# Optimization experiments

Measured on AMD Instinct MI355X. Metric: run time of the kernel, lower is better.

The kernel has to match this reference:

```python
import math
import jax, jax.numpy as jnp
import numpy as np

CHANNELS = 256
NUM_HEADS = 4
GROUPS = 32
EPS = 1e-5


def setup_inputs() -> dict:
    key = jax.random.key(0)
    ks = jax.random.split(key, 7)
    b, c, h, w = 8, CHANNELS, 48, 48
    return {
        "x": jax.random.normal(ks[0], (b, c, h, w), dtype=jnp.float32),
        "gn_w": jax.random.uniform(ks[1], (c,), dtype=jnp.float32),
        "gn_b": jax.random.normal(ks[2], (c,), dtype=jnp.float32) * 0.02,
        "qkv_w": jax.random.normal(ks[3], (3 * c, c), dtype=jnp.float32) * (1.0 / math.sqrt(c)),
        "qkv_b": jax.random.normal(ks[4], (3 * c,), dtype=jnp.float32) * 0.02,
        "proj_w": jax.random.normal(ks[5], (c, c), dtype=jnp.float32) * (1.0 / math.sqrt(c)),
        "proj_b": jax.random.normal(ks[6], (c,), dtype=jnp.float32) * 0.02,
    }


def reference(x, gn_w, gn_b, qkv_w, qkv_b, proj_w, proj_b):
    b, c, h, w = x.shape
    nh = NUM_HEADS
    hd = c // nh
    hw = h * w

    # GroupNorm(32, c): normalize over (c/G, h, w) per group
    xg = x.reshape(b, GROUPS, c // GROUPS, h, w)
    mean = jnp.mean(xg, axis=(2, 3, 4), keepdims=True)
    var = jnp.mean(jnp.square(xg - mean), axis=(2, 3, 4), keepdims=True)
    xn = (xg - mean) * jax.lax.rsqrt(var + EPS)
    xn = xn.reshape(b, c, h, w) * gn_w[None, :, None, None] + gn_b[None, :, None, None]

    # 1x1 conv qkv: per-pixel linear
    qkv = jnp.einsum('bchw,oc->bohw', xn, qkv_w) + qkv_b[None, :, None, None]
    q, k, v = jnp.split(qkv, 3, axis=1)  # each (b, c, h, w)

    # split channels into heads: (b, nh, hd, hw)
    q = q.reshape(b, nh, hd, hw)
    k = k.reshape(b, nh, hd, hw)
    v = v.reshape(b, nh, hd, hw)

    scale = 1.0 / math.sqrt(hd)
    attn = jnp.einsum('bndi,bndj->bnij', q, k) * scale  # (b, nh, hw, hw)
    attn = jax.nn.softmax(attn, axis=-1)
    out = jnp.einsum('bnij,bndj->bndi', attn, v)  # (b, nh, hd, hw)
    out = out.reshape(b, c, h, w)

    out = jnp.einsum('bchw,oc->bohw', out, proj_w) + proj_b[None, :, None, None]
    return x + out
```

## Files before the change

### kernel.cpp

```cpp
#include <hip/hip_runtime.h>
#include <hip/hip_bf16.h>
#include <math.h>

#define NB 8
#define NC 256
#define NHW 2304
#define NH 4
#define HD 64
#define CPG 8
#define GN_EPS 1e-5f

typedef __bf16 bf16;
typedef __bf16 bf16x4 __attribute__((ext_vector_type(4)));
typedef __bf16 bf16x8 __attribute__((ext_vector_type(8)));
typedef float f32x4 __attribute__((ext_vector_type(4)));
typedef float f32x16 __attribute__((ext_vector_type(16)));
typedef int i32x4 __attribute__((ext_vector_type(4)));
typedef unsigned int u32;

#define MFMA16(a, b, c) __builtin_amdgcn_mfma_f32_16x16x32_bf16(a, b, c, 0, 0, 0)
#define MFMA32(a, b, c) __builtin_amdgcn_mfma_f32_32x32x16_bf16(a, b, c, 0, 0, 0)

__global__ __launch_bounds__(256) void k_pre(const float* __restrict__ x,
                                             const float* __restrict__ gw,
                                             const float* __restrict__ gb,
                                             const float* __restrict__ qw,
                                             const float* __restrict__ pw,
                                             bf16* __restrict__ xnt,
                                             bf16* __restrict__ wq,
                                             bf16* __restrict__ wp) {
  int t = threadIdx.x;
  if (blockIdx.x < 768) {
    int i = blockIdx.x * 256 + t;
    wq[i] = (bf16)qw[i];
    if (i < NC * NC) wp[i] = (bf16)pw[i];
    return;
  }
  int bid = blockIdx.x - 768;
  int b = bid >> 5;
  int g = bid & 31;
  int c0 = g * CPG;
  const float* xb = x + (b * NC + c0) * NHW;
  float s = 0.f, s2 = 0.f;
  for (int p = t; p < NHW; p += 256) {
#pragma unroll
    for (int cc = 0; cc < CPG; ++cc) {
      float v = xb[cc * NHW + p];
      s += v;
      s2 += v * v;
    }
  }
#pragma unroll
  for (int m = 1; m < 64; m <<= 1) {
    s += __shfl_xor(s, m);
    s2 += __shfl_xor(s2, m);
  }
  __shared__ float red[8];
  int wid = t >> 6;
  if ((t & 63) == 0) { red[wid] = s; red[4 + wid] = s2; }
  __syncthreads();
  s = red[0] + red[1] + red[2] + red[3];
  s2 = red[4] + red[5] + red[6] + red[7];
  const float inv_n = 1.0f / (CPG * NHW);
  float mean = s * inv_n;
  float var = s2 * inv_n - mean * mean;
  float rsq = rsqrtf(var + GN_EPS);
  float ka[CPG], kb[CPG];
#pragma unroll
  for (int cc = 0; cc < CPG; ++cc) {
    float wv = gw[c0 + cc];
    ka[cc] = wv * rsq;
    kb[cc] = gb[c0 + cc] - mean * rsq * wv;
  }
  bf16* dst = xnt + b * NHW * NC + c0;
  for (int p = t; p < NHW; p += 256) {
    bf16x8 o;
#pragma unroll
    for (int cc = 0; cc < CPG; ++cc)
      o[cc] = (bf16)(xb[cc * NHW + p] * ka[cc] + kb[cc]);
    *reinterpret_cast<bf16x8*>(dst + p * NC) = o;
  }
}

__global__ __launch_bounds__(256) void k_qkv(const bf16* __restrict__ xnt,
                                             const bf16* __restrict__ wq,
                                             const float* __restrict__ qkvb,
                                             bf16* __restrict__ qt,
                                             bf16* __restrict__ kt,
                                             bf16* __restrict__ vv) {
  int b = blockIdx.z;
  int i_base = blockIdx.x * 128;
  int o_base = blockIdx.y * 128;
  int t = threadIdx.x;
  int lane = t & 63, wid = t >> 6;
  int wm = (wid >> 1) * 64, wn = (wid & 1) * 64;
  int l15 = lane & 15, g = lane >> 4;
  const bf16* ab = xnt + (b * NHW + i_base + wm + l15) * NC + g * 8;
  const bf16* bb = wq + (o_base + wn + l15) * NC + g * 8;
  f32x4 acc[4][4] = {};
#pragma unroll 2
  for (int kc = 0; kc < 8; ++kc) {
    bf16x8 af[4], bf[4];
#pragma unroll
    for (int mf = 0; mf < 4; ++mf)
      af[mf] = *reinterpret_cast<const bf16x8*>(ab + mf * 16 * NC + kc * 32);
#pragma unroll
    for (int nf = 0; nf < 4; ++nf)
      bf[nf] = *reinterpret_cast<const bf16x8*>(bb + nf * 16 * NC + kc * 32);
#pragma unroll
    for (int mf = 0; mf < 4; ++mf)
#pragma unroll
      for (int nf = 0; nf < 4; ++nf)
        acc[mf][nf] = MFMA16(af[mf], bf[nf], acc[mf][nf]);
  }
  int row0 = i_base + wm + g * 4;
  if (o_base + wn < 512) {
    const float qscale = 0.125f * 1.4426950408889634f;
#pragma unroll
    for (int nf = 0; nf < 4; ++nf) {
      int o = o_base + wn + nf * 16 + l15;
      float bias = qkvb[o];
      bf16* dst;
      float sc;
      int oo;
      if (o < 256) { dst = qt; sc = qscale; oo = o; }
      else         { dst = kt; sc = 1.0f;   oo = o - 256; }
      bf16* dp = dst + ((b * NH + (oo >> 6)) * NHW) * HD + (oo & 63);
#pragma unroll
      for (int mf = 0; mf < 4; ++mf)
#pragma unroll
        for (int r = 0; r < 4; ++r)
          dp[(row0 + mf * 16 + r) * HD] = (bf16)((acc[mf][nf][r] + bias) * sc);
    }
  } else {
#pragma unroll
    for (int nf = 0; nf < 4; ++nf) {
      int og = o_base + wn + nf * 16 + l15;
      float bias = qkvb[og];
      int o2 = og - 512;
      bf16* dp = vv + ((size_t)(b * NH + (o2 >> 6)) * HD + (o2 & 63)) * NHW +
                 i_base + wm + g * 4;
#pragma unroll
      for (int mf = 0; mf < 4; ++mf) {
        bf16x4 w;
#pragma unroll
        for (int r = 0; r < 4; ++r) w[r] = (bf16)(acc[mf][nf][r] + bias);
        *reinterpret_cast<bf16x4*>(dp + mf * 16) = w;
      }
    }
  }
}

__global__ __launch_bounds__(256) void k_attn(const bf16* __restrict__ qt,
                                              const bf16* __restrict__ kt,
                                              const bf16* __restrict__ vv,
                                              bf16* __restrict__ att) {
  __shared__ bf16 kbuf[2][64 * 64];
  __shared__ bf16 vbuf[2][64 * 64];

  const int bh = blockIdx.y;
  const int b = bh >> 2, n = bh & 3;
  const int tid = threadIdx.x;
  const int wid = tid >> 6, lane = tid & 63;
  const int l31 = lane & 31, g2 = lane >> 5;
  const int i0w = blockIdx.x * 128 + wid * 32;

  const bf16* qb = qt + (size_t)bh * NHW * HD;
  const bf16* kb = kt + (size_t)bh * NHW * HD;
  const bf16* vb = vv + (size_t)bh * HD * NHW;

  const int r0 = tid >> 3, cs = tid & 7;
  const bf16* kg0 = kb + r0 * HD + cs * 8;
  const bf16* kg1 = kb + (r0 + 32) * HD + cs * 8;
  const bf16* vg0 = vb + (size_t)r0 * NHW + cs * 8;
  const bf16* vg1 = vb + (size_t)(r0 + 32) * NHW + cs * 8;
  const int lw0 = r0 * 64 + ((cs ^ (r0 & 7)) * 8);
  const int lw1 = (r0 + 32) * 64 + ((cs ^ (r0 & 7)) * 8);

  const int foff = l31 * 64;
  int sw[4];
#pragma unroll
  for (int m = 0; m < 4; ++m) sw[m] = ((2 * m + g2) ^ (l31 & 7)) * 8;

  bf16x8 q[4];
#pragma unroll
  for (int kk = 0; kk < 4; ++kk)
    q[kk] = *reinterpret_cast<const bf16x8*>(qb + (i0w + l31) * HD + kk * 16 + g2 * 8);

  f32x16 acc0 = {}, acc1 = {};
  float l_r = 0.f;

  {
    bf16x8 a = *reinterpret_cast<const bf16x8*>(kg0);
    bf16x8 c = *reinterpret_cast<const bf16x8*>(kg1);
    bf16x8 d = *reinterpret_cast<const bf16x8*>(vg0);
    bf16x8 e = *reinterpret_cast<const bf16x8*>(vg1);
    *reinterpret_cast<bf16x8*>(&kbuf[0][lw0]) = a;
    *reinterpret_cast<bf16x8*>(&kbuf[0][lw1]) = c;
    *reinterpret_cast<bf16x8*>(&vbuf[0][lw0]) = d;
    *reinterpret_cast<bf16x8*>(&vbuf[0][lw1]) = e;
  }
  asm volatile("s_waitcnt lgkmcnt(0)" ::: "memory");
  __builtin_amdgcn_s_barrier();

  for (int t = 0; t < 36; ++t) {
    const int cur = t & 1;
    bf16x8 kr0, kr1, vr0, vr1;
    if (t < 35) {
      kr0 = *reinterpret_cast<const bf16x8*>(kg0 + (t + 1) * (64 * HD));
      kr1 = *reinterpret_cast<const bf16x8*>(kg1 + (t + 1) * (64 * HD));
      vr0 = *reinterpret_cast<const bf16x8*>(vg0 + (t + 1) * 64);
      vr1 = *reinterpret_cast<const bf16x8*>(vg1 + (t + 1) * 64);
    }
    const bf16* kc = kbuf[cur];
    const bf16* vc = vbuf[cur];

#pragma unroll
    for (int jt = 0; jt < 2; ++jt) {
      f32x16 s = {};
      __builtin_amdgcn_s_setprio(1);
#pragma unroll
      for (int kk = 0; kk < 4; ++kk) {
        bf16x8 kf = *reinterpret_cast<const bf16x8*>(kc + jt * 2048 + foff + sw[kk]);
        s = MFMA32(kf, q[kk], s);
      }
      __builtin_amdgcn_s_setprio(0);
      u32 P[8];
      float la = 0.f, lb = 0.f;
#pragma unroll
      for (int m = 0; m < 8; ++m) {
        float e0 = exp2f(s[2 * m]);
        float e1 = exp2f(s[2 * m + 1]);
        la += e0;
        lb += e1;
        u32 pk;
        asm("v_cvt_pk_bf16_f32 %0, %1, %2" : "=v"(pk) : "v"(e0), "v"(e1));
        P[m] = pk;
      }
      l_r += la + lb;
#pragma unroll
      for (int J = 0; J < 2; ++J) {
        u32 w0 = P[4 * J], w2 = P[4 * J + 2];
        asm("v_permlane32_swap_b32 %0, %1" : "+v"(w0), "+v"(w2));
        u32 w1 = P[4 * J + 1], w3 = P[4 * J + 3];
        asm("v_permlane32_swap_b32 %0, %1" : "+v"(w1), "+v"(w3));
        i32x4 wv;
        wv[0] = (int)w0; wv[1] = (int)w1; wv[2] = (int)w2; wv[3] = (int)w3;
        bf16x8 pf = __builtin_bit_cast(bf16x8, wv);
        const int jj = 2 * jt + J;
        bf16x8 v0 = *reinterpret_cast<const bf16x8*>(vc + foff + sw[jj]);
        bf16x8 v1 = *reinterpret_cast<const bf16x8*>(vc + 2048 + foff + sw[jj]);
        __builtin_amdgcn_s_setprio(1);
        acc0 = MFMA32(v0, pf, acc0);
        acc1 = MFMA32(v1, pf, acc1);
        __builtin_amdgcn_s_setprio(0);
      }
    }

    if (t < 35) {
      const int nb = cur ^ 1;
      *reinterpret_cast<bf16x8*>(&kbuf[nb][lw0]) = kr0;
      *reinterpret_cast<bf16x8*>(&kbuf[nb][lw1]) = kr1;
      *reinterpret_cast<bf16x8*>(&vbuf[nb][lw0]) = vr0;
      *reinterpret_cast<bf16x8*>(&vbuf[nb][lw1]) = vr1;
    }
    asm volatile("s_waitcnt lgkmcnt(0)" ::: "memory");
    __builtin_amdgcn_s_barrier();
  }

  l_r += __shfl_xor(l_r, 32);
  const float inv = 1.0f / l_r;
  bf16* ob = att + ((size_t)(b * NHW) + i0w + l31) * NC + n * HD;
#pragma unroll
  for (int rq = 0; rq < 4; ++rq) {
    bf16x4 o0, o1;
#pragma unroll
    for (int c = 0; c < 4; ++c) {
      o0[c] = (bf16)(acc0[rq * 4 + c] * inv);
      o1[c] = (bf16)(acc1[rq * 4 + c] * inv);
    }
    *reinterpret_cast<bf16x4*>(ob + 8 * rq + 4 * g2) = o0;
    *reinterpret_cast<bf16x4*>(ob + 32 + 8 * rq + 4 * g2) = o1;
  }
}

__global__ __launch_bounds__(256) void k_proj(const bf16* __restrict__ att,
                                              const bf16* __restrict__ wp,
                                              const float* __restrict__ pb,
                                              const float* __restrict__ x,
                                              float* __restrict__ out) {
  int b = blockIdx.z;
  int i_base = blockIdx.x * 128;
  int o_base = blockIdx.y * 128;
  int t = threadIdx.x;
  int lane = t & 63, wid = t >> 6;
  int wm = (wid >> 1) * 64, wn = (wid & 1) * 64;
  int l15 = lane & 15, g = lane >> 4;
  const bf16* ab = wp + (o_base + wm + l15) * NC + g * 8;
  const bf16* bb = att + (b * NHW + i_base + wn + l15) * NC + g * 8;
  f32x4 acc[4][4] = {};
#pragma unroll 2
  for (int kc = 0; kc < 8; ++kc) {
    bf16x8 af[4], bf[4];
#pragma unroll
    for (int mf = 0; mf < 4; ++mf)
      af[mf] = *reinterpret_cast<const bf16x8*>(ab + mf * 16 * NC + kc * 32);
#pragma unroll
    for (int nf = 0; nf < 4; ++nf)
      bf[nf] = *reinterpret_cast<const bf16x8*>(bb + nf * 16 * NC + kc * 32);
#pragma unroll
    for (int mf = 0; mf < 4; ++mf)
#pragma unroll
      for (int nf = 0; nf < 4; ++nf)
        acc[mf][nf] = MFMA16(af[mf], bf[nf], acc[mf][nf]);
  }
  int orow0 = o_base + wm + g * 4;
#pragma unroll
  for (int mf = 0; mf < 4; ++mf)
#pragma unroll
    for (int r = 0; r < 4; ++r) {
      int o = orow0 + mf * 16 + r;
      float bias = pb[o];
      const float* xr = x + (b * NC + o) * NHW + i_base + wn;
      float* orow = out + (b * NC + o) * NHW + i_base + wn;
#pragma unroll
      for (int nf = 0; nf < 4; ++nf) {
        int i = nf * 16 + l15;
        orow[i] = acc[mf][nf][r] + bias + xr[i];
      }
    }
}

extern "C" void kernel_launch(void* const* d_in, const int* in_sizes, int n_in,
                              void* d_out, int out_size, void* d_ws, size_t ws_size,
                              hipStream_t stream) {
  const float* x    = (const float*)d_in[0];
  const float* gnw  = (const float*)d_in[1];
  const float* gnb  = (const float*)d_in[2];
  const float* qkvw = (const float*)d_in[3];
  const float* qkvb = (const float*)d_in[4];
  const float* pw   = (const float*)d_in[5];
  const float* pb   = (const float*)d_in[6];
  float* out = (float*)d_out;

  bf16* ws = (bf16*)d_ws;
  const size_t NE = (size_t)NB * NHW * NC;
  bf16* xnt = ws;
  bf16* qt  = ws + NE;
  bf16* kt  = ws + 2 * NE;
  bf16* vv  = ws + 3 * NE;
  bf16* att = ws + 4 * NE;
  bf16* wqb = ws + 5 * NE;
  bf16* wpb = wqb + 768 * 256;

  k_pre<<<1024, 256, 0, stream>>>(x, gnw, gnb, qkvw, pw, xnt, wqb, wpb);
  k_qkv<<<dim3(18, 6, NB), 256, 0, stream>>>(xnt, wqb, qkvb, qt, kt, vv);
  k_attn<<<dim3(18, 32), 256, 0, stream>>>(qt, kt, vv, att);
  k_proj<<<dim3(18, 2, NB), 256, 0, stream>>>(att, wpb, pb, x, out);
}
```

Baseline: 169.2 us.

## Split attention KV range across waves, read K/V directly from global, vectorize QK stores

The attention kernel now processes 64 query rows per block, with two wave pairs each covering half of the key range. Partial accumulators are combined through a small shared-memory reduction. K and V fragments are read directly from global memory (relying on cache) instead of through a double-buffered LDS pipeline with barriers. The grid is flattened to 1152 blocks with an XCD-aware remap. The QKV GEMM also swaps operands for Q/K outputs so it can write bf16x4 vector stores instead of scalar strided stores. This adds more blocks and drops per-tile barriers, at the risk of more global/L2 traffic for K/V reads.

Result: slower. 248.8 us (+47.0%).

```diff
diff --git a/kernel.cpp b/kernel.cpp
--- a/kernel.cpp
+++ b/kernel.cpp
@@ -95,8 +95,16 @@
   int lane = t & 63, wid = t >> 6;
   int wm = (wid >> 1) * 64, wn = (wid & 1) * 64;
   int l15 = lane & 15, g = lane >> 4;
-  const bf16* ab = xnt + (b * NHW + i_base + wm + l15) * NC + g * 8;
-  const bf16* bb = wq + (o_base + wn + l15) * NC + g * 8;
+  const bool qk = (o_base < 512);
+  const bf16* ab;
+  const bf16* bb;
+  if (qk) {
+    ab = wq + (o_base + wm + l15) * NC + g * 8;
+    bb = xnt + ((size_t)b * NHW + i_base + wn + l15) * NC + g * 8;
+  } else {
+    ab = xnt + ((size_t)b * NHW + i_base + wm + l15) * NC + g * 8;
+    bb = wq + (o_base + wn + l15) * NC + g * 8;
+  }
   f32x4 acc[4][4] = {};
 #pragma unroll 2
   for (int kc = 0; kc < 8; ++kc) {
@@ -113,24 +121,26 @@
       for (int nf = 0; nf < 4; ++nf)
         acc[mf][nf] = MFMA16(af[mf], bf[nf], acc[mf][nf]);
   }
-  int row0 = i_base + wm + g * 4;
-  if (o_base + wn < 512) {
+  if (qk) {
     const float qscale = 0.125f * 1.4426950408889634f;
 #pragma unroll
-    for (int nf = 0; nf < 4; ++nf) {
-      int o = o_base + wn + nf * 16 + l15;
-      float bias = qkvb[o];
-      bf16* dst;
-      float sc;
-      int oo;
-      if (o < 256) { dst = qt; sc = qscale; oo = o; }
-      else         { dst = kt; sc = 1.0f;   oo = o - 256; }
-      bf16* dp = dst + ((b * NH + (oo >> 6)) * NHW) * HD + (oo & 63);
-#pragma unroll
-      for (int mf = 0; mf < 4; ++mf)
+    for (int mf = 0; mf < 4; ++mf) {
+      int o0 = o_base + wm + mf * 16 + g * 4;
+      f32x4 b4 = *reinterpret_cast<const f32x4*>(qkvb + o0);
+      bool isQ = (o0 < 256);
+      float sc = isQ ? qscale : 1.0f;
+      int oo = isQ ? o0 : o0 - 256;
+      bf16* base = (isQ ? qt : kt) +
+                   ((size_t)(b * NH + (oo >> 6)) * NHW) * HD + (oo & 63);
+#pragma unroll
+      for (int nf = 0; nf < 4; ++nf) {
+        int i = i_base + wn + nf * 16 + l15;
+        bf16x4 w;
 #pragma unroll
         for (int r = 0; r < 4; ++r)
-          dp[(row0 + mf * 16 + r) * HD] = (bf16)((acc[mf][nf][r] + bias) * sc);
+          w[r] = (bf16)((acc[mf][nf][r] + b4[r]) * sc);
+        *reinterpret_cast<bf16x4*>(base + (size_t)i * HD) = w;
+      }
     }
   } else {
 #pragma unroll
@@ -151,77 +161,49 @@
   }
 }
 
-__global__ __launch_bounds__(256) void k_attn(const bf16* __restrict__ qt,
-                                              const bf16* __restrict__ kt,
-                                              const bf16* __restrict__ vv,
-                                              bf16* __restrict__ att) {
-  __shared__ bf16 kbuf[2][64 * 64];
-  __shared__ bf16 vbuf[2][64 * 64];
-
-  const int bh = blockIdx.y;
-  const int b = bh >> 2, n = bh & 3;
+__global__ __launch_bounds__(256, 4) void k_attn(const bf16* __restrict__ qt,
+                                                 const bf16* __restrict__ kt,
+                                                 const bf16* __restrict__ vv,
+                                                 bf16* __restrict__ att) {
+  __shared__ float mbuf[2][64][33];
+
   const int tid = threadIdx.x;
   const int wid = tid >> 6, lane = tid & 63;
   const int l31 = lane & 31, g2 = lane >> 5;
-  const int i0w = blockIdx.x * 128 + wid * 32;
+  const int ig = wid & 1, jh = wid >> 1;
+
+  const int bid = blockIdx.x;
+  const int wg = (bid & 7) * 144 + (bid >> 3);
+  const int bh = wg / 36, it = wg % 36;
+  const int b = bh >> 2, n = bh & 3;
+  const int i0 = it * 64 + ig * 32;
 
   const bf16* qb = qt + (size_t)bh * NHW * HD;
   const bf16* kb = kt + (size_t)bh * NHW * HD;
   const bf16* vb = vv + (size_t)bh * HD * NHW;
 
-  const int r0 = tid >> 3, cs = tid & 7;
-  const bf16* kg0 = kb + r0 * HD + cs * 8;
-  const bf16* kg1 = kb + (r0 + 32) * HD + cs * 8;
-  const bf16* vg0 = vb + (size_t)r0 * NHW + cs * 8;
-  const bf16* vg1 = vb + (size_t)(r0 + 32) * NHW + cs * 8;
-  const int lw0 = r0 * 64 + ((cs ^ (r0 & 7)) * 8);
-  const int lw1 = (r0 + 32) * 64 + ((cs ^ (r0 & 7)) * 8);
-
-  const int foff = l31 * 64;
-  int sw[4];
-#pragma unroll
-  for (int m = 0; m < 4; ++m) sw[m] = ((2 * m + g2) ^ (l31 & 7)) * 8;
-
   bf16x8 q[4];
 #pragma unroll
   for (int kk = 0; kk < 4; ++kk)
-    q[kk] = *reinterpret_cast<const bf16x8*>(qb + (i0w + l31) * HD + kk * 16 + g2 * 8);
+    q[kk] = *reinterpret_cast<const bf16x8*>(qb + (i0 + l31) * HD + kk * 16 + g2 * 8);
+
+  const bf16* kR = kb + (size_t)(jh * 1152 + l31) * HD + g2 * 8;
+  const bf16* vR0 = vb + (size_t)l31 * NHW + jh * 1152 + g2 * 8;
+  const bf16* vR1 = vR0 + (size_t)32 * NHW;
 
   f32x16 acc0 = {}, acc1 = {};
   float l_r = 0.f;
 
-  {
-    bf16x8 a = *reinterpret_cast<const bf16x8*>(kg0);
-    bf16x8 c = *reinterpret_cast<const bf16x8*>(kg1);
-    bf16x8 d = *reinterpret_cast<const bf16x8*>(vg0);
-    bf16x8 e = *reinterpret_cast<const bf16x8*>(vg1);
-    *reinterpret_cast<bf16x8*>(&kbuf[0][lw0]) = a;
-    *reinterpret_cast<bf16x8*>(&kbuf[0][lw1]) = c;
-    *reinterpret_cast<bf16x8*>(&vbuf[0][lw0]) = d;
-    *reinterpret_cast<bf16x8*>(&vbuf[0][lw1]) = e;
-  }
-  asm volatile("s_waitcnt lgkmcnt(0)" ::: "memory");
-  __builtin_amdgcn_s_barrier();
-
-  for (int t = 0; t < 36; ++t) {
-    const int cur = t & 1;
-    bf16x8 kr0, kr1, vr0, vr1;
-    if (t < 35) {
-      kr0 = *reinterpret_cast<const bf16x8*>(kg0 + (t + 1) * (64 * HD));
-      kr1 = *reinterpret_cast<const bf16x8*>(kg1 + (t + 1) * (64 * HD));
-      vr0 = *reinterpret_cast<const bf16x8*>(vg0 + (t + 1) * 64);
-      vr1 = *reinterpret_cast<const bf16x8*>(vg1 + (t + 1) * 64);
-    }
-    const bf16* kc = kbuf[cur];
-    const bf16* vc = vbuf[cur];
-
+  for (int t = 0; t < 18; ++t) {
+    const int jb = t * 64;
 #pragma unroll
     for (int jt = 0; jt < 2; ++jt) {
       f32x16 s = {};
       __builtin_amdgcn_s_setprio(1);
 #pragma unroll
       for (int kk = 0; kk < 4; ++kk) {
-        bf16x8 kf = *reinterpret_cast<const bf16x8*>(kc + jt * 2048 + foff + sw[kk]);
+        bf16x8 kf = *reinterpret_cast<const bf16x8*>(
+            kR + (size_t)(jb + jt * 32) * HD + kk * 16);
         s = MFMA32(kf, q[kk], s);
       }
       __builtin_amdgcn_s_setprio(0);
@@ -248,39 +230,42 @@
         wv[0] = (int)w0; wv[1] = (int)w1; wv[2] = (int)w2; wv[3] = (int)w3;
         bf16x8 pf = __builtin_bit_cast(bf16x8, wv);
         const int jj = 2 * jt + J;
-        bf16x8 v0 = *reinterpret_cast<const bf16x8*>(vc + foff + sw[jj]);
-        bf16x8 v1 = *reinterpret_cast<const bf16x8*>(vc + 2048 + foff + sw[jj]);
+        bf16x8 v0 = *reinterpret_cast<const bf16x8*>(vR0 + jb + jj * 16);
+        bf16x8 v1 = *reinterpret_cast<const bf16x8*>(vR1 + jb + jj * 16);
         __builtin_amdgcn_s_setprio(1);
         acc0 = MFMA32(v0, pf, acc0);
         acc1 = MFMA32(v1, pf, acc1);
         __builtin_amdgcn_s_setprio(0);
       }
     }
-
-    if (t < 35) {
-      const int nb = cur ^ 1;
-      *reinterpret_cast<bf16x8*>(&kbuf[nb][lw0]) = kr0;
-      *reinterpret_cast<bf16x8*>(&kbuf[nb][lw1]) = kr1;
-      *reinterpret_cast<bf16x8*>(&vbuf[nb][lw0]) = vr0;
-      *reinterpret_cast<bf16x8*>(&vbuf[nb][lw1]) = vr1;
-    }
-    asm volatile("s_waitcnt lgkmcnt(0)" ::: "memory");
-    __builtin_amdgcn_s_barrier();
-  }
-
-  l_r += __shfl_xor(l_r, 32);
-  const float inv = 1.0f / l_r;
-  bf16* ob = att + ((size_t)(b * NHW) + i0w + l31) * NC + n * HD;
-#pragma unroll
-  for (int rq = 0; rq < 4; ++rq) {
-    bf16x4 o0, o1;
-#pragma unroll
-    for (int c = 0; c < 4; ++c) {
-      o0[c] = (bf16)(acc0[rq * 4 + c] * inv);
-      o1[c] = (bf16)(acc1[rq * 4 + c] * inv);
-    }
-    *reinterpret_cast<bf16x4*>(ob + 8 * rq + 4 * g2) = o0;
-    *reinterpret_cast<bf16x4*>(ob + 32 + 8 * rq + 4 * g2) = o1;
+  }
+
+  if (jh == 1) {
+    float* mb = mbuf[ig][lane];
+#pragma unroll
+    for (int e = 0; e < 16; ++e) { mb[e] = acc0[e]; mb[16 + e] = acc1[e]; }
+    mb[32] = l_r;
+  }
+  __syncthreads();
+  if (jh == 0) {
+    const float* mb = mbuf[ig][lane];
+#pragma unroll
+    for (int e = 0; e < 16; ++e) { acc0[e] += mb[e]; acc1[e] += mb[16 + e]; }
+    l_r += mb[32];
+    l_r += __shfl_xor(l_r, 32);
+    const float inv = 1.0f / l_r;
+    bf16* ob = att + ((size_t)(b * NHW) + i0 + l31) * NC + n * HD;
+#pragma unroll
+    for (int rq = 0; rq < 4; ++rq) {
+      bf16x4 o0, o1;
+#pragma unroll
+      for (int c = 0; c < 4; ++c) {
+        o0[c] = (bf16)(acc0[rq * 4 + c] * inv);
+        o1[c] = (bf16)(acc1[rq * 4 + c] * inv);
+      }
+      *reinterpret_cast<bf16x4*>(ob + 8 * rq + 4 * g2) = o0;
+      *reinterpret_cast<bf16x4*>(ob + 32 + 8 * rq + 4 * g2) = o1;
+    }
   }
 }
 
@@ -355,6 +340,6 @@
 
   k_pre<<<1024, 256, 0, stream>>>(x, gnw, gnb, qkvw, pw, xnt, wqb, wpb);
   k_qkv<<<dim3(18, 6, NB), 256, 0, stream>>>(xnt, wqb, qkvb, qt, kt, vv);
-  k_attn<<<dim3(18, 32), 256, 0, stream>>>(qt, kt, vv, att);
+  k_attn<<<1152, 256, 0, stream>>>(qt, kt, vv, att);
   k_proj<<<dim3(18, 2, NB), 256, 0, stream>>>(att, wpb, pb, x, out);
 }
```
